# Kernel tuning notes

Measured on AMD Instinct MI355X. Metric: run time of the kernel, lower is better.

## Reference

```python
import jax, jax.numpy as jnp
import numpy as np

N, F_IN, C0, C1, H, E, G = 50000, 128, 64, 64, 4, 800000, 256
NEG_SLOPE = 0.2
BN_EPS = 1e-5


def setup_inputs() -> dict:
    key = jax.random.key(0)
    ks = jax.random.split(key, 16)
    d = {
        'x': jax.random.normal(ks[0], (N, F_IN), dtype=jnp.float32),
        'edge_index': jax.random.randint(ks[1], (2, E), 0, N, dtype=jnp.int64),
        'batch': jnp.sort(jax.random.randint(ks[2], (N,), 0, G, dtype=jnp.int64)),
        # conv1 params
        'W1': jax.random.normal(ks[3], (F_IN, H * C0), dtype=jnp.float32) * (1.0 / np.sqrt(F_IN)),
        'att_src1': jax.random.normal(ks[4], (H, C0), dtype=jnp.float32) * 0.1,
        'att_dst1': jax.random.normal(ks[5], (H, C0), dtype=jnp.float32) * 0.1,
        'b1': jnp.zeros((H * C0,), dtype=jnp.float32),
        # batchnorm params
        'gamma': jnp.ones((H * C0,), dtype=jnp.float32),
        'beta': jnp.zeros((H * C0,), dtype=jnp.float32),
        # conv2 params
        'W2': jax.random.normal(ks[6], (H * C0, H * C1), dtype=jnp.float32) * (1.0 / np.sqrt(H * C0)),
        'att_src2': jax.random.normal(ks[7], (H, C1), dtype=jnp.float32) * 0.1,
        'att_dst2': jax.random.normal(ks[8], (H, C1), dtype=jnp.float32) * 0.1,
        'b2': jnp.zeros((H * C1,), dtype=jnp.float32),
    }
    return d


def _gat_layer(x, W, a_src, a_dst, b, src, dst, heads, ch):
    # x: [N, Fin] -> h: [N, H, C]
    h = (x @ W).reshape(N, heads, ch)
    al_src = jnp.sum(h * a_src, axis=-1)  # [N, H]
    al_dst = jnp.sum(h * a_dst, axis=-1)  # [N, H]
    e = jax.nn.leaky_relu(al_src[src] + al_dst[dst], NEG_SLOPE)  # [E', H]
    m = jax.ops.segment_max(e, dst, num_segments=N)
    m = jnp.where(jnp.isfinite(m), m, 0.0)
    ex = jnp.exp(e - m[dst])
    denom = jax.ops.segment_sum(ex, dst, num_segments=N)
    alpha = ex / (denom[dst] + 1e-16)  # softmax over in-neighborhood of dst
    out = jax.ops.segment_sum(alpha[:, :, None] * h[src], dst, num_segments=N)  # [N, H, C]
    return out.reshape(N, heads * ch) + b


def _batchnorm(x, gamma, beta):
    mu = jnp.mean(x, axis=0)
    var = jnp.var(x, axis=0)
    return gamma * (x - mu) / jnp.sqrt(var + BN_EPS) + beta


def reference(x, edge_index, batch, W1, att_src1, att_dst1, b1, gamma, beta,
              W2, att_src2, att_dst2, b2):
    # add self loops (PyG GATConv default)
    loops = jnp.arange(N, dtype=edge_index.dtype)
    src = jnp.concatenate([edge_index[0], loops])
    dst = jnp.concatenate([edge_index[1], loops])

    x1 = _gat_layer(x, W1, att_src1, att_dst1, b1, src, dst, H, C0)
    x1 = jax.nn.relu(_batchnorm(x1, gamma, beta))
    x2 = jax.nn.relu(_gat_layer(x1, W2, att_src2, att_dst2, b2, src, dst, H, C1))

    xc = jnp.concatenate([x1, x2], axis=1)  # [N, H*C0 + H*C1]
    counts = jax.ops.segment_sum(jnp.ones((N,), xc.dtype), batch, num_segments=G)
    x_mean = jax.ops.segment_sum(xc, batch, num_segments=G) / jnp.maximum(counts, 1.0)[:, None]
    x_max = jax.ops.segment_max(xc, batch, num_segments=G)
    x_max = jnp.where(jnp.isfinite(x_max), x_max, 0.0)
    return jnp.concatenate([x_mean, x_max], axis=1)  # [G, 2*(H*C0+H*C1)]
```

## Files before the change

kernel.cpp:

```cpp
#include <hip/hip_runtime.h>
#include <hip/hip_bf16.h>
#include <hip/hip_fp16.h>
#include <math.h>

#define NN 50000
#define FIN 128
#define FH 256
#define NE 800000
#define NG 256
#define ELLS 64
#define NEG_SLOPE 0.2f
#define BN_EPS 1e-5f

typedef short bf16x8 __attribute__((ext_vector_type(8)));
typedef unsigned short u16x8 __attribute__((ext_vector_type(8)));
typedef unsigned long long u64x2 __attribute__((ext_vector_type(2)));
typedef float f32x4 __attribute__((ext_vector_type(4)));
typedef _Float16 f16x8 __attribute__((ext_vector_type(8)));

__device__ __forceinline__ float lrelu(float x) { return x > 0.f ? x : NEG_SLOPE * x; }
__device__ __forceinline__ float bf2f(unsigned short u) { return __uint_as_float(((unsigned int)u) << 16); }
__device__ __forceinline__ unsigned short f2bf(float f) {
    __hip_bfloat16 b = __float2bfloat16(f);
    return *reinterpret_cast<unsigned short*>(&b);
}
__device__ __forceinline__ unsigned short f2h(float f) {
    __half h = __float2half(f);
    return *reinterpret_cast<unsigned short*>(&h);
}
__device__ __forceinline__ float h2f(unsigned short u) {
    __half_raw r; r.x = u;
    return __half2float(__half(r));
}

__global__ __launch_bounds__(256) void k_prep(const float* __restrict__ W1, unsigned short* __restrict__ W1t,
                                              const float* __restrict__ W2, unsigned short* __restrict__ W2t,
                                              int* __restrict__ cnt, int* __restrict__ colIdx) {
    int bid = blockIdx.x;
    if (bid < 384) {
        int o = bid * 256 + threadIdx.x;
        if (o < 256 * 128) {
            int c = o >> 7, k = o & 127;
            W1t[o] = f2bf(W1[(size_t)k * 256 + c]);
        } else {
            o -= 256 * 128;
            if (o < 256 * 256) {
                int c = o >> 8, k = o & 255;
                W2t[o] = f2bf(W2[(size_t)k * 256 + c]);
            }
        }
    } else {
        int i = (bid - 384) * 256 + threadIdx.x;
        if (i < NN) {
            cnt[i] = 1;
            colIdx[(size_t)i * ELLS] = i;
        }
    }
}

template<int MODE>
__global__ __launch_bounds__(256) void k_gemm(const float* __restrict__ Af, const unsigned short* __restrict__ Ab,
                                              const unsigned short* __restrict__ Bt,
                                              unsigned short* __restrict__ C,
                                              const float* __restrict__ attS, const float* __restrict__ attD,
                                              float* __restrict__ alsrc, float* __restrict__ aldst,
                                              const float* __restrict__ bnsum, const float* __restrict__ bnsq,
                                              const float* __restrict__ gamma, const float* __restrict__ beta,
                                              const int* __restrict__ eiFill, int* __restrict__ cntFill,
                                              int* __restrict__ colIdxFill, int nGemm, int nFill,
                                              int M, int K) {
    __shared__ short lds[10240];
    __shared__ float sAs_[128], sAd_[128];
    __shared__ float s_scale[MODE == 1 ? 256 : 1];
    __shared__ float s_shift[MODE == 1 ? 256 : 1];
    short* As = lds;
    short* Bs = lds + 5120;

    int bid = blockIdx.x;
    if (MODE == 0 && bid >= nGemm) {
        int T = nFill * 256;
        int t = (bid - nGemm) * 256 + threadIdx.x;
        int s[8], d[8], p[8];
#pragma unroll
        for (int k = 0; k < 8; ++k) {
            int e = t + k * T;
            if (e < NE) { s[k] = eiFill[e]; d[k] = eiFill[NE + e]; } else { s[k] = 0; d[k] = -1; }
        }
#pragma unroll
        for (int k = 0; k < 8; ++k)
            p[k] = (d[k] >= 0) ? atomicAdd(&cntFill[d[k]], 1) : 0;
#pragma unroll
        for (int k = 0; k < 8; ++k)
            if (d[k] >= 0 && p[k] < ELLS) colIdxFill[(size_t)d[k] * ELLS + p[k]] = s[k];
        return;
    }
    int tid = threadIdx.x;
    int lane = tid & 63, wid = tid >> 6;
    int wr = wid >> 1, wc = wid & 1;
    int row0 = (bid >> 1) * 128, col0 = (bid & 1) * 128;

    if (tid < 128) {
        sAs_[tid] = attS[col0 + tid];
        sAd_[tid] = attD[col0 + tid];
    }
    if (MODE == 1) {
        const float invN = 1.f / (float)NN;
        float mean = bnsum[tid] * invN;
        float var  = bnsq[tid] * invN - mean * mean;
        float istd = rsqrtf(var + BN_EPS);
        float sc = gamma[tid] * istd;
        s_scale[tid] = sc;
        s_shift[tid] = beta[tid] - mean * sc;
        __syncthreads();
    }
    f32x4 acc[4][4];
#pragma unroll
    for (int m = 0; m < 4; ++m)
#pragma unroll
        for (int n = 0; n < 4; ++n) acc[m][n] = (f32x4){0.f, 0.f, 0.f, 0.f};

    int r = tid >> 2, seg = tid & 3;
    int koff = (lane >> 4) * 8;

    float4 qa0[2], qa1[2];
    bf16x8 qab[2];
    bf16x8 qb[2];
    const float4 zf4 = make_float4(0.f, 0.f, 0.f, 0.f);
    const bf16x8 zb8 = {0, 0, 0, 0, 0, 0, 0, 0};

#pragma unroll
    for (int j = 0; j < 2; ++j) {
        int grow = row0 + r + j * 64;
        if (MODE == 0) {
            if (grow < M) {
                const float* ap = Af + (size_t)grow * K + seg * 8;
                qa0[j] = *(const float4*)ap;
                qa1[j] = *((const float4*)ap + 1);
            } else { qa0[j] = zf4; qa1[j] = zf4; }
        } else {
            qab[j] = (grow < M) ? *(const bf16x8*)(Ab + (size_t)grow * K + seg * 8) : zb8;
        }
        qb[j] = *(const bf16x8*)(Bt + (size_t)(col0 + r + j * 64) * K + seg * 8);
    }

    for (int k0 = 0; k0 < K; k0 += 32) {
#pragma unroll
        for (int j = 0; j < 2; ++j) {
            int row = r + j * 64;
            bf16x8 va;
            if (MODE == 0) {
                va[0] = (short)f2bf(qa0[j].x); va[1] = (short)f2bf(qa0[j].y);
                va[2] = (short)f2bf(qa0[j].z); va[3] = (short)f2bf(qa0[j].w);
                va[4] = (short)f2bf(qa1[j].x); va[5] = (short)f2bf(qa1[j].y);
                va[6] = (short)f2bf(qa1[j].z); va[7] = (short)f2bf(qa1[j].w);
            } else {
                int cb = k0 + seg * 8;
#pragma unroll
                for (int k = 0; k < 8; ++k) {
                    float f = bf2f((unsigned short)qab[j][k]) * s_scale[cb + k] + s_shift[cb + k];
                    va[k] = (short)f2bf(fmaxf(f, 0.f));
                }
            }
            *(bf16x8*)&As[row * 40 + seg * 8] = va;
            *(bf16x8*)&Bs[row * 40 + seg * 8] = qb[j];
        }
        __syncthreads();
        int kn = k0 + 32;
        if (kn < K) {
#pragma unroll
            for (int j = 0; j < 2; ++j) {
                int grow = row0 + r + j * 64;
                if (MODE == 0) {
                    if (grow < M) {
                        const float* ap = Af + (size_t)grow * K + kn + seg * 8;
                        qa0[j] = *(const float4*)ap;
                        qa1[j] = *((const float4*)ap + 1);
                    } else { qa0[j] = zf4; qa1[j] = zf4; }
                } else {
                    qab[j] = (grow < M) ? *(const bf16x8*)(Ab + (size_t)grow * K + kn + seg * 8) : zb8;
                }
                qb[j] = *(const bf16x8*)(Bt + (size_t)(col0 + r + j * 64) * K + kn + seg * 8);
            }
        }
        bf16x8 af[4], bfr[4];
#pragma unroll
        for (int m = 0; m < 4; ++m)
            af[m] = *(const bf16x8*)&As[(wr * 64 + m * 16 + (lane & 15)) * 40 + koff];
#pragma unroll
        for (int n = 0; n < 4; ++n)
            bfr[n] = *(const bf16x8*)&Bs[(wc * 64 + n * 16 + (lane & 15)) * 40 + koff];
#pragma unroll
        for (int m = 0; m < 4; ++m)
#pragma unroll
            for (int n = 0; n < 4; ++n)
                acc[m][n] = __builtin_amdgcn_mfma_f32_16x16x32_bf16(af[m], bfr[n], acc[m][n], 0, 0, 0);
        __syncthreads();
    }

    const int CST = 138;
#pragma unroll 1
    for (int hh = 0; hh < 2; ++hh) {
        if (wr == hh) {
#pragma unroll
            for (int m = 0; m < 4; ++m) {
                int rl = m * 16 + (lane >> 4) * 4;
#pragma unroll
                for (int n = 0; n < 4; ++n) {
                    int cl = wc * 64 + n * 16 + (lane & 15);
#pragma unroll
                    for (int j = 0; j < 4; ++j)
                        lds[(rl + j) * CST + cl] = (short)f2h(acc[m][n][j]);
                }
            }
        }
        __syncthreads();
        int rl = tid >> 2, q = tid & 3;
        int grow = row0 + hh * 64 + rl;
        if (grow < M) {
            const short* cp = &lds[rl * CST + q * 32];
            bf16x8 v0 = *(const bf16x8*)(cp + 0);
            bf16x8 v1 = *(const bf16x8*)(cp + 8);
            bf16x8 v2 = *(const bf16x8*)(cp + 16);
            bf16x8 v3 = *(const bf16x8*)(cp + 24);
            unsigned short* op = C + (size_t)grow * 256 + col0 + q * 32;
            *(bf16x8*)(op + 0)  = v0;
            *(bf16x8*)(op + 8)  = v1;
            *(bf16x8*)(op + 16) = v2;
            *(bf16x8*)(op + 24) = v3;
            float ps = 0.f, pd = 0.f;
            const float* aS = &sAs_[q * 32];
            const float* aD = &sAd_[q * 32];
#pragma unroll
            for (int k = 0; k < 8; ++k) {
                float f0 = h2f((unsigned short)v0[k]);
                float f1 = h2f((unsigned short)v1[k]);
                float f2 = h2f((unsigned short)v2[k]);
                float f3 = h2f((unsigned short)v3[k]);
                ps += f0 * aS[k] + f1 * aS[k + 8] + f2 * aS[k + 16] + f3 * aS[k + 24];
                pd += f0 * aD[k] + f1 * aD[k + 8] + f2 * aD[k + 16] + f3 * aD[k + 24];
            }
            ps += __shfl_xor(ps, 1);
            pd += __shfl_xor(pd, 1);
            if ((q & 1) == 0) {
                int head = (col0 >> 6) + (q >> 1);
                alsrc[grow * 4 + head] = ps;
                aldst[grow * 4 + head] = pd;
            }
        }
        __syncthreads();
    }
}

__global__ __launch_bounds__(256) void k_gat_agg(const int* __restrict__ cnt, const int* __restrict__ colIdx,
    const float* __restrict__ alsrc, const float* __restrict__ aldst, const unsigned short* __restrict__ h,
    const float* __restrict__ bias, unsigned short* __restrict__ outb, int relu_nt, int n) {
    __shared__ float ex_s[4][2][32][4];
    __shared__ int   src_s[4][2][32];
    int wave = threadIdx.x >> 6, lane = threadIdx.x & 63;
    int half = lane >> 5, hlane = lane & 31;
    int node = blockIdx.x * 8 + wave * 2 + half;
    int deg = min(cnt[node], ELLS);
    const int* crow = colIdx + (size_t)node * ELLS;
    int hf = hlane >> 3;
    float4 ad = *(const float4*)(aldst + (size_t)node * 4);
    float m0 = -1e30f, m1 = -1e30f, m2 = -1e30f, m3 = -1e30f;
    float d0 = 0.f, d1 = 0.f, d2 = 0.f, d3 = 0.f;
    f16x8 accv = {0, 0, 0, 0, 0, 0, 0, 0};
    const f16x8 zh8 = {0, 0, 0, 0, 0, 0, 0, 0};

    for (int base = 0; base < deg; base += 32) {
        int cnt32 = min(32, deg - base);
        int src = node;
        float e0 = -1e30f, e1 = -1e30f, e2 = -1e30f, e3 = -1e30f;
        if (hlane < cnt32) {
            src = crow[base + hlane];
            float4 as = *(const float4*)(alsrc + (size_t)src * 4);
            e0 = lrelu(as.x + ad.x);
            e1 = lrelu(as.y + ad.y);
            e2 = lrelu(as.z + ad.z);
            e3 = lrelu(as.w + ad.w);
        }
        float c0 = e0, c1 = e1, c2 = e2, c3 = e3;
#pragma unroll
        for (int off = 16; off > 0; off >>= 1) {
            c0 = fmaxf(c0, __shfl_xor(c0, off));
            c1 = fmaxf(c1, __shfl_xor(c1, off));
            c2 = fmaxf(c2, __shfl_xor(c2, off));
            c3 = fmaxf(c3, __shfl_xor(c3, off));
        }
        float nm0 = fmaxf(m0, c0), nm1 = fmaxf(m1, c1), nm2 = fmaxf(m2, c2), nm3 = fmaxf(m3, c3);
        float sc0 = __expf(m0 - nm0), sc1 = __expf(m1 - nm1), sc2 = __expf(m2 - nm2), sc3 = __expf(m3 - nm3);
        float x0 = __expf(e0 - nm0), x1 = __expf(e1 - nm1), x2 = __expf(e2 - nm2), x3 = __expf(e3 - nm3);
        float s0 = x0, s1 = x1, s2 = x2, s3 = x3;
#pragma unroll
        for (int off = 16; off > 0; off >>= 1) {
            s0 += __shfl_xor(s0, off);
            s1 += __shfl_xor(s1, off);
            s2 += __shfl_xor(s2, off);
            s3 += __shfl_xor(s3, off);
        }
        d0 = d0 * sc0 + s0; d1 = d1 * sc1 + s1; d2 = d2 * sc2 + s2; d3 = d3 * sc3 + s3;
        m0 = nm0; m1 = nm1; m2 = nm2; m3 = nm3;
        float scl = (hf == 0) ? sc0 : (hf == 1) ? sc1 : (hf == 2) ? sc2 : sc3;
        {
            _Float16 sh = (_Float16)scl;
            f16x8 sv = {sh, sh, sh, sh, sh, sh, sh, sh};
            accv *= sv;
        }
        ex_s[wave][half][hlane][0] = x0; ex_s[wave][half][hlane][1] = x1;
        ex_s[wave][half][hlane][2] = x2; ex_s[wave][half][hlane][3] = x3;
        src_s[wave][half][hlane] = src;
        for (int j = 0; j < cnt32; j += 4) {
            f16x8 hv[4];
            float w[4];
#pragma unroll
            for (int u = 0; u < 4; ++u) {
                if (j + u < cnt32) {
                    w[u] = ex_s[wave][half][j + u][hf];
                    hv[u] = *(const f16x8*)(h + (size_t)src_s[wave][half][j + u] * 256 + hlane * 8);
                } else { w[u] = 0.f; hv[u] = zh8; }
            }
#pragma unroll
            for (int u = 0; u < 4; ++u) {
                _Float16 wh = (_Float16)w[u];
                f16x8 wv = {wh, wh, wh, wh, wh, wh, wh, wh};
                accv += hv[u] * wv;
            }
        }
    }

    float dd = (hf == 0) ? d0 : (hf == 1) ? d1 : (hf == 2) ? d2 : d3;
    float inv = 1.f / (dd + 1e-16f);
    float4 b0 = *(const float4*)(bias + hlane * 8);
    float4 b1 = *(const float4*)(bias + hlane * 8 + 4);
    float o[8];
    o[0] = (float)accv[0] * inv + b0.x; o[1] = (float)accv[1] * inv + b0.y;
    o[2] = (float)accv[2] * inv + b0.z; o[3] = (float)accv[3] * inv + b0.w;
    o[4] = (float)accv[4] * inv + b1.x; o[5] = (float)accv[5] * inv + b1.y;
    o[6] = (float)accv[6] * inv + b1.z; o[7] = (float)accv[7] * inv + b1.w;
    u16x8 ob;
    if (relu_nt) {
#pragma unroll
        for (int k = 0; k < 8; ++k) ob[k] = f2bf(fmaxf(o[k], 0.f));
        u64x2 w = *(u64x2*)&ob;
        __builtin_nontemporal_store(w, (u64x2*)(outb + (size_t)node * 256 + hlane * 8));
    } else {
#pragma unroll
        for (int k = 0; k < 8; ++k) ob[k] = f2bf(o[k]);
        *(u64x2*)(outb + (size_t)node * 256 + hlane * 8) = *(u64x2*)&ob;
    }
}

__global__ __launch_bounds__(256) void k_bn_stats(const unsigned short* __restrict__ xin, float* bnsum, float* bnsq) {
    __shared__ float ls[8][256], lq[8][256];
    int t = threadIdx.x, cg = t & 31, rg = t >> 5;
    int r0 = blockIdx.x * 200;
    float s[8], q[8];
#pragma unroll
    for (int k = 0; k < 8; ++k) { s[k] = 0.f; q[k] = 0.f; }
    for (int r = r0 + rg; r < r0 + 200; r += 8) {
        u16x8 v = *(const u16x8*)(xin + (size_t)r * 256 + cg * 8);
#pragma unroll
        for (int k = 0; k < 8; ++k) {
            float f = bf2f(v[k]);
            s[k] += f; q[k] += f * f;
        }
    }
#pragma unroll
    for (int k = 0; k < 8; ++k) { ls[rg][cg * 8 + k] = s[k]; lq[rg][cg * 8 + k] = q[k]; }
    __syncthreads();
    float S = 0.f, Q = 0.f;
#pragma unroll
    for (int j = 0; j < 8; ++j) { S += ls[j][t]; Q += lq[j][t]; }
    atomicAdd(&bnsum[t], S);
    atomicAdd(&bnsq[t], Q);
}

__global__ __launch_bounds__(512) void k_pool(const unsigned short* __restrict__ x1pre,
    const unsigned short* __restrict__ x2b, const int* __restrict__ batch,
    const float* __restrict__ bnsum, const float* __restrict__ bnsq,
    const float* __restrict__ gamma, const float* __restrict__ beta,
    float* __restrict__ out) {
    int g = blockIdx.x;
    __shared__ int sLo, sHi;
    if (threadIdx.x == 0) {
        int lo = 0, hi = NN;
        while (lo < hi) { int m = (lo + hi) >> 1; if (batch[m] < g) lo = m + 1; else hi = m; }
        sLo = lo;
    }
    if (threadIdx.x == 1) {
        int lo = 0, hi = NN;
        while (lo < hi) { int m = (lo + hi) >> 1; if (batch[m] < g + 1) lo = m + 1; else hi = m; }
        sHi = lo;
    }
    __syncthreads();
    int lo = sLo, hi = sHi, cnt = hi - lo;
    int t = threadIdx.x;
    bool first = t < 256;
    int f = first ? t : t - 256;
    const unsigned short* src = first ? x1pre : x2b;
    float sc = 1.f, sh = 0.f;
    if (first) {
        const float invN = 1.f / (float)NN;
        float mean = bnsum[f] * invN;
        float var  = bnsq[f] * invN - mean * mean;
        float istd = rsqrtf(var + BN_EPS);
        sc = gamma[f] * istd;
        sh = beta[f] - mean * sc;
    }
    float s = 0.f, mx = 0.f;
    int r = lo;
    for (; r + 1 < hi; r += 2) {
        float va = bf2f(src[(size_t)r * 256 + f]);
        float vb = bf2f(src[(size_t)(r + 1) * 256 + f]);
        if (first) {
            va = fmaxf(va * sc + sh, 0.f);
            vb = fmaxf(vb * sc + sh, 0.f);
        }
        s += va + vb;
        mx = fmaxf(mx, fmaxf(va, vb));
    }
    if (r < hi) {
        float va = bf2f(src[(size_t)r * 256 + f]);
        if (first) va = fmaxf(va * sc + sh, 0.f);
        s += va; mx = fmaxf(mx, va);
    }
    float mean = (cnt > 0) ? s / (float)cnt : 0.f;
    int off = first ? 0 : 256;
    out[g * 1024 + off + f] = mean;
    out[g * 1024 + 512 + off + f] = mx;
}

extern "C" void kernel_launch(void* const* d_in, const int* in_sizes, int n_in,
                              void* d_out, int out_size, void* d_ws, size_t ws_size,
                              hipStream_t stream) {
    const float* x     = (const float*)d_in[0];
    const int*   ei    = (const int*)d_in[1];
    const int*   batch = (const int*)d_in[2];
    const float* W1    = (const float*)d_in[3];
    const float* asrc1 = (const float*)d_in[4];
    const float* adst1 = (const float*)d_in[5];
    const float* b1    = (const float*)d_in[6];
    const float* gamma = (const float*)d_in[7];
    const float* beta  = (const float*)d_in[8];
    const float* W2    = (const float*)d_in[9];
    const float* asrc2 = (const float*)d_in[10];
    const float* adst2 = (const float*)d_in[11];
    const float* b2    = (const float*)d_in[12];
    float* out = (float*)d_out;

    char* p = (char*)d_ws;
    auto alloc = [&](size_t bytes) -> void* {
        void* r = (void*)p;
        p += (bytes + 255) & ~(size_t)255;
        return r;
    };
    unsigned short* hb    = (unsigned short*)alloc((size_t)NN * 256 * 2);
    unsigned short* x1pre = (unsigned short*)alloc((size_t)NN * 256 * 2);
    unsigned short* x2b   = (unsigned short*)alloc((size_t)NN * 256 * 2);
    unsigned short* W1t   = (unsigned short*)alloc((size_t)256 * 128 * 2);
    unsigned short* W2t   = (unsigned short*)alloc((size_t)256 * 256 * 2);
    float* alsrc = (float*)alloc((size_t)NN * 4 * 4);
    float* aldst = (float*)alloc((size_t)NN * 4 * 4);
    float* bnsum = (float*)alloc(256 * 4);
    float* bnsq  = (float*)alloc(256 * 4);
    int*   cnt   = (int*)alloc((size_t)NN * 4);
    int*   colIdx = (int*)alloc((size_t)NN * ELLS * 4);

    (void)hipMemsetAsync(bnsum, 0, 2 * 1024, stream);

    const int nGemm = 2 * ((NN + 127) / 128);
    const int nFill = (NE / 8 + 255) / 256;

    k_prep<<<384 + 196, 256, 0, stream>>>(W1, W1t, W2, W2t, cnt, colIdx);

    k_gemm<0><<<nGemm + nFill, 256, 0, stream>>>(x, nullptr, W1t, hb, asrc1, adst1, alsrc, aldst,
                                                 nullptr, nullptr, nullptr, nullptr,
                                                 ei, cnt, colIdx, nGemm, nFill, NN, 128);
    k_gat_agg<<<NN / 8, 256, 0, stream>>>(cnt, colIdx, alsrc, aldst, hb, b1, x1pre, 0, NN);
    k_bn_stats<<<250, 256, 0, stream>>>(x1pre, bnsum, bnsq);

    k_gemm<1><<<nGemm, 256, 0, stream>>>(nullptr, x1pre, W2t, hb, asrc2, adst2, alsrc, aldst,
                                         bnsum, bnsq, gamma, beta,
                                         nullptr, nullptr, nullptr, nGemm, 0, NN, 256);
    k_gat_agg<<<NN / 8, 256, 0, stream>>>(cnt, colIdx, alsrc, aldst, hb, b2, x2b, 1, NN);

    k_pool<<<NG, 512, 0, stream>>>(x1pre, x2b, batch, bnsum, bnsq, gamma, beta, out);
}
```

Baseline: 287.3 us.

## Sort nodes by in-degree before GAT aggregation to balance wave work

Adds a degree histogram and a counting-sort pass that builds a node order from highest to lowest in-degree. Both aggregation kernels then map each half-wave to a node through this order, so the two nodes sharing a wave have similar degree and per-wave loop counts are more uniform. The cost is two extra small kernel launches with atomics, plus output writes and row reads that become scattered rather than sequential by node.

```diff
diff --git a/kernel.cpp b/kernel.cpp
--- a/kernel.cpp
+++ b/kernel.cpp
@@ -55,6 +55,28 @@
             cnt[i] = 1;
             colIdx[(size_t)i * ELLS] = i;
         }
+    }
+}
+
+__global__ void k_hist(const int* __restrict__ cnt, int* __restrict__ bins) {
+    int i = blockIdx.x * 256 + threadIdx.x;
+    if (i < NN) atomicAdd(&bins[min(cnt[i], ELLS)], 1);
+}
+__global__ __launch_bounds__(256) void k_order(const int* __restrict__ cnt, const int* __restrict__ bins,
+                                               int* __restrict__ cursor, int* __restrict__ order) {
+    __shared__ int start[ELLS + 1];
+    int t = threadIdx.x;
+    if (t <= ELLS) {
+        int s = 0;
+        for (int k = ELLS; k > t; --k) s += bins[k];
+        start[t] = s;
+    }
+    __syncthreads();
+    int i = blockIdx.x * 256 + t;
+    if (i < NN) {
+        int dg = min(cnt[i], ELLS);
+        int pos = atomicAdd(&cursor[dg], 1);
+        order[start[dg] + pos] = i;
     }
 }
 
@@ -251,14 +273,15 @@
     }
 }
 
-__global__ __launch_bounds__(256) void k_gat_agg(const int* __restrict__ cnt, const int* __restrict__ colIdx,
+__global__ __launch_bounds__(256) void k_gat_agg(const int* __restrict__ order, const int* __restrict__ cnt,
+    const int* __restrict__ colIdx,
     const float* __restrict__ alsrc, const float* __restrict__ aldst, const unsigned short* __restrict__ h,
     const float* __restrict__ bias, unsigned short* __restrict__ outb, int relu_nt, int n) {
     __shared__ float ex_s[4][2][32][4];
     __shared__ int   src_s[4][2][32];
     int wave = threadIdx.x >> 6, lane = threadIdx.x & 63;
     int half = lane >> 5, hlane = lane & 31;
-    int node = blockIdx.x * 8 + wave * 2 + half;
+    int node = order[blockIdx.x * 8 + wave * 2 + half];
     int deg = min(cnt[node], ELLS);
     const int* crow = colIdx + (size_t)node * ELLS;
     int hf = hlane >> 3;
@@ -464,11 +487,15 @@
     float* aldst = (float*)alloc((size_t)NN * 4 * 4);
     float* bnsum = (float*)alloc(256 * 4);
     float* bnsq  = (float*)alloc(256 * 4);
+    int*   bins   = (int*)alloc(128 * 4);
+    int*   cursor = (int*)alloc(128 * 4);
     int*   cnt   = (int*)alloc((size_t)NN * 4);
+    int*   order = (int*)alloc((size_t)NN * 4);
     int*   colIdx = (int*)alloc((size_t)NN * ELLS * 4);
 
-    (void)hipMemsetAsync(bnsum, 0, 2 * 1024, stream);
-
+    (void)hipMemsetAsync(bnsum, 0, 3 * 1024, stream);
+
+    const int nb196 = (NN + 255) / 256;
     const int nGemm = 2 * ((NN + 127) / 128);
     const int nFill = (NE / 8 + 255) / 256;
 
@@ -477,13 +504,16 @@
     k_gemm<0><<<nGemm + nFill, 256, 0, stream>>>(x, nullptr, W1t, hb, asrc1, adst1, alsrc, aldst,
                                                  nullptr, nullptr, nullptr, nullptr,
                                                  ei, cnt, colIdx, nGemm, nFill, NN, 128);
-    k_gat_agg<<<NN / 8, 256, 0, stream>>>(cnt, colIdx, alsrc, aldst, hb, b1, x1pre, 0, NN);
+    k_hist<<<nb196, 256, 0, stream>>>(cnt, bins);
+    k_order<<<nb196, 256, 0, stream>>>(cnt, bins, cursor, order);
+
+    k_gat_agg<<<NN / 8, 256, 0, stream>>>(order, cnt, colIdx, alsrc, aldst, hb, b1, x1pre, 0, NN);
     k_bn_stats<<<250, 256, 0, stream>>>(x1pre, bnsum, bnsq);
 
     k_gemm<1><<<nGemm, 256, 0, stream>>>(nullptr, x1pre, W2t, hb, asrc2, adst2, alsrc, aldst,
                                          bnsum, bnsq, gamma, beta,
                                          nullptr, nullptr, nullptr, nGemm, 0, NN, 256);
-    k_gat_agg<<<NN / 8, 256, 0, stream>>>(cnt, colIdx, alsrc, aldst, hb, b2, x2b, 1, NN);
+    k_gat_agg<<<NN / 8, 256, 0, stream>>>(order, cnt, colIdx, alsrc, aldst, hb, b2, x2b, 1, NN);
 
     k_pool<<<NG, 512, 0, stream>>>(x1pre, x2b, batch, bnsum, bnsq, gamma, beta, out);
 }
```

After: 564.0 us. +96.3%, slower.
